# Performance work log

Measured on AMD Instinct MI355X. Metric: run time of the kernel, lower is better.

Reference implementation:

```python
import jax, jax.numpy as jnp
import numpy as np

N, IN_DIM, NUM_HEADS, HEAD_DIM = 8192, 256, 4, 64
NEG_SLOPE = 0.2


def setup_inputs() -> dict:
    key = jax.random.key(0)
    k1, k2, k3, k4 = jax.random.split(key, 4)
    h = jax.random.normal(k1, (N, IN_DIM), dtype=jnp.float32)
    adj = jax.random.randint(k2, (N, N), 0, 2, dtype=jnp.int32)
    # xavier-ish init scale for the per-head projection weights and attention vector
    W = jax.random.normal(k3, (NUM_HEADS, IN_DIM, HEAD_DIM), dtype=jnp.float32) * (1.0 / np.sqrt(IN_DIM))
    a = jax.random.normal(k4, (2 * HEAD_DIM, 1), dtype=jnp.float32) * (1.0 / np.sqrt(2 * HEAD_DIM))
    return {"h": h, "adj": adj, "W": W, "a": a}


def reference(h, adj, W, a):
    # Wh: (H, N, D) -- per-head linear projection (no bias)
    Wh = jnp.einsum('ni,hid->hnd', h, W)
    # torch computes cat([Wh_i, Wh_j]) @ a; equivalent decomposition:
    # e_ij = (Wh_i . a[:D]) + (Wh_j . a[D:])  -- avoids the O(N^2 * 2D) concat tensor
    a1 = a[:HEAD_DIM, 0]  # (D,)
    a2 = a[HEAD_DIM:, 0]  # (D,)
    s_i = jnp.einsum('hnd,d->hn', Wh, a1)  # (H, N)
    s_j = jnp.einsum('hnd,d->hn', Wh, a2)  # (H, N)
    e = s_i[:, :, None] + s_j[:, None, :]  # (H, N, N)
    e = jnp.where(e > 0, e, NEG_SLOPE * e)  # leaky_relu(0.2)
    e = jnp.where(adj[None, :, :] == 0, -jnp.inf, e)
    att = jax.nn.softmax(e, axis=-1)  # torch softmax(dim=1) over last axis of (N,N)
    # dropout is identity in eval mode
    out = jnp.einsum('hnm,hmd->hnd', att, Wh)  # (H, N, D)
    # concat head outputs along feature dim -> (N, H*D)
    return jnp.transpose(out, (1, 0, 2)).reshape(N, NUM_HEADS * HEAD_DIM)
```

## Files before the change

kernel.cpp:

```cpp
#include <hip/hip_runtime.h>
#include <hip/hip_bf16.h>

#define NND 8192

typedef __attribute__((ext_vector_type(8))) __bf16 bf16x8;
typedef __attribute__((ext_vector_type(4))) float f32x4;
typedef __attribute__((ext_vector_type(4))) unsigned int u32x4;
typedef __attribute__((ext_vector_type(2))) unsigned int u32x2;

__global__ __launch_bounds__(256) void gat_phase0(
    const int* __restrict__ adj, unsigned long long* __restrict__ bits)
{
  const int wave = threadIdx.x >> 6, lane = threadIdx.x & 63;
  const int row = blockIdx.x * 4 + wave;
  const int* ap = adj + (size_t)row * NND + lane;
  unsigned long long* bp = bits + (size_t)row * 128;
  #pragma unroll 4
  for (int it = 0; it < 128; ++it) {
    int v = ap[it * 64];
    unsigned long long m = __ballot(v != 0);
    if (lane == 0) bp[it] = m;
  }
}

__global__ __launch_bounds__(256) void gat_phase1a(
    const float* __restrict__ W, const float* __restrict__ av,
    float* __restrict__ q1, float* __restrict__ q2)
{
  const int t = blockIdx.x * 256 + threadIdx.x;
  const float* wp = W + (size_t)t * 64;
  float p1 = 0.f, p2 = 0.f;
  #pragma unroll
  for (int d = 0; d < 64; d += 4) {
    f32x4 w  = *(const f32x4*)(wp + d);
    f32x4 a1 = *(const f32x4*)(av + d);
    f32x4 a2 = *(const f32x4*)(av + 64 + d);
    p1 += w[0]*a1[0] + w[1]*a1[1] + w[2]*a1[2] + w[3]*a1[3];
    p2 += w[0]*a2[0] + w[1]*a2[1] + w[2]*a2[2] + w[3]*a2[3];
  }
  q1[t] = p1 * 1.4426950408889634f;
  q2[t] = p2 * 1.4426950408889634f;
}

__global__ __launch_bounds__(1024) void gat_phase1(
    const float* __restrict__ hin, const float* __restrict__ W,
    const float* __restrict__ q1, const float* __restrict__ q2,
    float* __restrict__ s1, float* __restrict__ s2, unsigned int* __restrict__ whbF)
{
  const int t = threadIdx.x;
  const int wave = t >> 6, lane = t & 63;
  const int head = wave & 3, dt = wave >> 2;
  const int lo = lane & 15, kg = lane >> 4;
  const float* Wp = W + head * 16384 + dt * 16 + lo;
  bf16x8 wf[8];
  #pragma unroll
  for (int ks = 0; ks < 8; ++ks)
    #pragma unroll
    for (int e = 0; e < 8; ++e)
      wf[ks][e] = (__bf16)Wp[(ks * 32 + kg * 8 + e) * 64];
  const float* q1h = q1 + head * 256;
  const float* q2h = q2 + head * 256;

  #pragma unroll
  for (int c = 0; c < 2; ++c) {
    const int n0 = blockIdx.x * 32 + c * 16;
    const float* hrow = hin + (size_t)(n0 + lo) * 256;
    f32x4 acc = (f32x4)(0.f);
    float p1 = 0.f, p2 = 0.f;
    #pragma unroll
    for (int ks = 0; ks < 8; ++ks) {
      const int kb = ks * 32 + kg * 8;
      f32x4 h0 = *(const f32x4*)(hrow + kb);
      f32x4 h1 = *(const f32x4*)(hrow + kb + 4);
      bf16x8 hf;
      #pragma unroll
      for (int e = 0; e < 4; ++e) { hf[e] = (__bf16)h0[e]; hf[e + 4] = (__bf16)h1[e]; }
      acc = __builtin_amdgcn_mfma_f32_16x16x32_bf16(hf, wf[ks], acc, 0, 0, 0);
      if (dt == 0) {
        f32x4 qa = *(const f32x4*)(q1h + kb);
        f32x4 qb = *(const f32x4*)(q1h + kb + 4);
        f32x4 qc = *(const f32x4*)(q2h + kb);
        f32x4 qd = *(const f32x4*)(q2h + kb + 4);
        #pragma unroll
        for (int e = 0; e < 4; ++e) {
          p1 = fmaf(h0[e], qa[e], p1); p1 = fmaf(h1[e], qb[e], p1);
          p2 = fmaf(h0[e], qc[e], p2); p2 = fmaf(h1[e], qd[e], p2);
        }
      }
    }
    const int jtg = n0 >> 6, sub = (n0 >> 4) & 3;
    const int chunk = ((head * 4 + dt) * 128 + jtg) * 2 + (kg >> 1);
    unsigned short b0 = __builtin_bit_cast(unsigned short, (__bf16)acc[0]);
    unsigned short b1 = __builtin_bit_cast(unsigned short, (__bf16)acc[1]);
    unsigned short b2 = __builtin_bit_cast(unsigned short, (__bf16)acc[2]);
    unsigned short b3 = __builtin_bit_cast(unsigned short, (__bf16)acc[3]);
    u32x2 wv; wv[0] = (unsigned)b0 | ((unsigned)b1 << 16);
    wv[1] = (unsigned)b2 | ((unsigned)b3 << 16);
    *(u32x2*)(whbF + (size_t)chunk * 256 + (sub * 16 + lo) * 4 + (kg & 1) * 2) = wv;
    if (dt == 0) {
      p1 += __shfl_xor(p1, 16, 64); p1 += __shfl_xor(p1, 32, 64);
      p2 += __shfl_xor(p2, 16, 64); p2 += __shfl_xor(p2, 32, 64);
      if (kg == 0) { s1[head * NND + n0 + lo] = p1; s2[head * NND + n0 + lo] = p2; }
    }
  }
}

__global__ __launch_bounds__(1024) void gat_phase2(
    const unsigned long long* __restrict__ bits, const float* __restrict__ s1,
    const float* __restrict__ s2, const unsigned short* __restrict__ whbF,
    float* __restrict__ out)
{
  __shared__ float red[4][64][44];
  const int t = threadIdx.x;
  const int wave = t >> 6, lane = t & 63;
  const int head = wave & 3, jseg = wave >> 2;
  const int i0 = blockIdx.x * 32;
  const int lo = lane & 15, kg = lane >> 4;
  const float s1v0 = s1[head * NND + i0 + lo];
  const float s1v1 = s1[head * NND + i0 + 16 + lo];
  const unsigned char* br0 = (const unsigned char*)bits + (size_t)(i0 + lo) * 1024 + kg * 2;
  const unsigned char* br1 = br0 + 16 * 1024;
  const float* s2h = s2 + head * NND;
  const char* wfb = (const char*)whbF + (size_t)head * 1048576 + (size_t)lane * 16;
  f32x4 acc0[4], acc1[4], dn0 = (f32x4)(0.f), dn1 = (f32x4)(0.f);
  #pragma unroll
  for (int dt = 0; dt < 4; ++dt) { acc0[dt] = (f32x4)(0.f); acc1[dt] = (f32x4)(0.f); }
  bf16x8 ones;
  #pragma unroll
  for (int e = 0; e < 8; ++e) ones[e] = (__bf16)1.0f;

  auto mkaf = [&](float s1v, unsigned m, f32x4 sa, f32x4 sb, int bb) -> bf16x8 {
    bf16x8 af;
    #pragma unroll
    for (int e = 0; e < 4; ++e) {
      float x = s1v + sa[e];
      x = fmaxf(x, 0.2f * x);
      float w = __builtin_amdgcn_exp2f(x);
      w = ((m >> (bb + e)) & 1u) ? w : 0.0f;
      af[e] = (__bf16)w;
    }
    #pragma unroll
    for (int e = 0; e < 4; ++e) {
      float x = s1v + sb[e];
      x = fmaxf(x, 0.2f * x);
      float w = __builtin_amdgcn_exp2f(x);
      w = ((m >> (bb + 4 + e)) & 1u) ? w : 0.0f;
      af[e + 4] = (__bf16)w;
    }
    return af;
  };

  #pragma unroll 2
  for (int jt = 0; jt < 32; ++jt) {
    const int jtg = jseg * 32 + jt;
    const int j0 = jtg * 64;
    u32x4 bb[8];
    #pragma unroll
    for (int dt = 0; dt < 4; ++dt)
      #pragma unroll
      for (int ks = 0; ks < 2; ++ks)
        bb[dt * 2 + ks] = *(const u32x4*)(wfb + dt * 262144 + jtg * 2048 + ks * 1024);
    const unsigned m0 = *(const unsigned short*)(br0 + (j0 >> 3));
    const unsigned m1 = *(const unsigned short*)(br1 + (j0 >> 3));
    const f32x4 sv0 = *(const f32x4*)(s2h + j0 + kg * 16);
    const f32x4 sv1 = *(const f32x4*)(s2h + j0 + kg * 16 + 4);
    const f32x4 sv2 = *(const f32x4*)(s2h + j0 + kg * 16 + 8);
    const f32x4 sv3 = *(const f32x4*)(s2h + j0 + kg * 16 + 12);
    {
      bf16x8 af = mkaf(s1v0, m0, sv0, sv1, 0);
      acc0[0] = __builtin_amdgcn_mfma_f32_16x16x32_bf16(af, __builtin_bit_cast(bf16x8, bb[0]), acc0[0], 0, 0, 0);
      acc0[1] = __builtin_amdgcn_mfma_f32_16x16x32_bf16(af, __builtin_bit_cast(bf16x8, bb[2]), acc0[1], 0, 0, 0);
      acc0[2] = __builtin_amdgcn_mfma_f32_16x16x32_bf16(af, __builtin_bit_cast(bf16x8, bb[4]), acc0[2], 0, 0, 0);
      acc0[3] = __builtin_amdgcn_mfma_f32_16x16x32_bf16(af, __builtin_bit_cast(bf16x8, bb[6]), acc0[3], 0, 0, 0);
      dn0 = __builtin_amdgcn_mfma_f32_16x16x32_bf16(af, ones, dn0, 0, 0, 0);
      af = mkaf(s1v0, m0, sv2, sv3, 8);
      acc0[0] = __builtin_amdgcn_mfma_f32_16x16x32_bf16(af, __builtin_bit_cast(bf16x8, bb[1]), acc0[0], 0, 0, 0);
      acc0[1] = __builtin_amdgcn_mfma_f32_16x16x32_bf16(af, __builtin_bit_cast(bf16x8, bb[3]), acc0[1], 0, 0, 0);
      acc0[2] = __builtin_amdgcn_mfma_f32_16x16x32_bf16(af, __builtin_bit_cast(bf16x8, bb[5]), acc0[2], 0, 0, 0);
      acc0[3] = __builtin_amdgcn_mfma_f32_16x16x32_bf16(af, __builtin_bit_cast(bf16x8, bb[7]), acc0[3], 0, 0, 0);
      dn0 = __builtin_amdgcn_mfma_f32_16x16x32_bf16(af, ones, dn0, 0, 0, 0);
    }
    {
      bf16x8 af = mkaf(s1v1, m1, sv0, sv1, 0);
      acc1[0] = __builtin_amdgcn_mfma_f32_16x16x32_bf16(af, __builtin_bit_cast(bf16x8, bb[0]), acc1[0], 0, 0, 0);
      acc1[1] = __builtin_amdgcn_mfma_f32_16x16x32_bf16(af, __builtin_bit_cast(bf16x8, bb[2]), acc1[1], 0, 0, 0);
      acc1[2] = __builtin_amdgcn_mfma_f32_16x16x32_bf16(af, __builtin_bit_cast(bf16x8, bb[4]), acc1[2], 0, 0, 0);
      acc1[3] = __builtin_amdgcn_mfma_f32_16x16x32_bf16(af, __builtin_bit_cast(bf16x8, bb[6]), acc1[3], 0, 0, 0);
      dn1 = __builtin_amdgcn_mfma_f32_16x16x32_bf16(af, ones, dn1, 0, 0, 0);
      af = mkaf(s1v1, m1, sv2, sv3, 8);
      acc1[0] = __builtin_amdgcn_mfma_f32_16x16x32_bf16(af, __builtin_bit_cast(bf16x8, bb[1]), acc1[0], 0, 0, 0);
      acc1[1] = __builtin_amdgcn_mfma_f32_16x16x32_bf16(af, __builtin_bit_cast(bf16x8, bb[3]), acc1[1], 0, 0, 0);
      acc1[2] = __builtin_amdgcn_mfma_f32_16x16x32_bf16(af, __builtin_bit_cast(bf16x8, bb[5]), acc1[2], 0, 0, 0);
      acc1[3] = __builtin_amdgcn_mfma_f32_16x16x32_bf16(af, __builtin_bit_cast(bf16x8, bb[7]), acc1[3], 0, 0, 0);
      dn1 = __builtin_amdgcn_mfma_f32_16x16x32_bf16(af, ones, dn1, 0, 0, 0);
    }
  }

  for (int s = 1; s <= 3; ++s) {
    if (jseg == s) {
      #pragma unroll
      for (int dt = 0; dt < 4; ++dt) {
        *(f32x4*)&red[head][lane][dt * 4] = acc0[dt];
        *(f32x4*)&red[head][lane][16 + dt * 4] = acc1[dt];
      }
      *(f32x4*)&red[head][lane][32] = dn0;
      *(f32x4*)&red[head][lane][36] = dn1;
    }
    __syncthreads();
    if (jseg == 0) {
      #pragma unroll
      for (int dt = 0; dt < 4; ++dt) {
        acc0[dt] += *(const f32x4*)&red[head][lane][dt * 4];
        acc1[dt] += *(const f32x4*)&red[head][lane][16 + dt * 4];
      }
      dn0 += *(const f32x4*)&red[head][lane][32];
      dn1 += *(const f32x4*)&red[head][lane][36];
    }
    __syncthreads();
  }
  if (jseg != 0) return;

  #pragma unroll
  for (int r = 0; r < 4; ++r) {
    const float rc0 = 1.0f / dn0[r], rc1 = 1.0f / dn1[r];
    float* op0 = out + (size_t)(i0 + kg * 4 + r) * 256 + head * 64 + lo;
    float* op1 = op0 + 16 * 256;
    #pragma unroll
    for (int dt = 0; dt < 4; ++dt) {
      op0[dt * 16] = acc0[dt][r] * rc0;
      op1[dt * 16] = acc1[dt][r] * rc1;
    }
  }
}

extern "C" void kernel_launch(void* const* d_in, const int* in_sizes, int n_in,
                              void* d_out, int out_size, void* d_ws, size_t ws_size,
                              hipStream_t stream) {
  const float* h   = (const float*)d_in[0];
  const int*   adj = (const int*)d_in[1];
  const float* W   = (const float*)d_in[2];
  const float* a   = (const float*)d_in[3];
  float* out = (float*)d_out;
  float* s1 = (float*)d_ws;
  float* s2 = s1 + 4 * NND;
  float* q1 = s2 + 4 * NND;
  float* q2 = q1 + 1024;
  unsigned long long* bits = (unsigned long long*)(q2 + 1024);
  unsigned int* whbF = (unsigned int*)(bits + (size_t)NND * 128);
  gat_phase0<<<dim3(NND / 4), dim3(256), 0, stream>>>(adj, bits);
  gat_phase1a<<<dim3(4), dim3(256), 0, stream>>>(W, a, q1, q2);
  gat_phase1<<<dim3(NND / 32), dim3(1024), 0, stream>>>(h, W, q1, q2, s1, s2, whbF);
  gat_phase2<<<dim3(NND / 32), dim3(1024), 0, stream>>>(bits, s1, s2, (const unsigned short*)whbF, out);
}
```

Before: 564.4 us.

## Remove split-j reduction in attention kernel, add register double-buffering, rework projection

The attention kernel no longer splits the neighbor dimension across four wave groups and reduces partial sums through shared memory. Each wave now handles 16 rows over all 8192 columns with a software-pipelined double buffer of register tiles, and blocks shrink to 512 threads. This removes the LDS reduction and barriers and halves per-wave accumulator registers, but each wave now loops four times longer and the masks and Wh tiles are reloaded per 16-row group instead of shared across 32 rows. The projection kernel is also reorganized: one wave per head computes all four feature tiles from register-held h fragments, and blocks shrink to 256 threads.

After: 542.1 us. -4.0%, faster.

```diff
diff --git a/kernel.cpp b/kernel.cpp
--- a/kernel.cpp
+++ b/kernel.cpp
@@ -42,53 +42,55 @@
   q2[t] = p2 * 1.4426950408889634f;
 }
 
-__global__ __launch_bounds__(1024) void gat_phase1(
+__global__ __launch_bounds__(256) void gat_phase1(
     const float* __restrict__ hin, const float* __restrict__ W,
     const float* __restrict__ q1, const float* __restrict__ q2,
     float* __restrict__ s1, float* __restrict__ s2, unsigned int* __restrict__ whbF)
 {
   const int t = threadIdx.x;
-  const int wave = t >> 6, lane = t & 63;
-  const int head = wave & 3, dt = wave >> 2;
+  const int head = t >> 6, lane = t & 63;
   const int lo = lane & 15, kg = lane >> 4;
-  const float* Wp = W + head * 16384 + dt * 16 + lo;
-  bf16x8 wf[8];
-  #pragma unroll
-  for (int ks = 0; ks < 8; ++ks)
-    #pragma unroll
-    for (int e = 0; e < 8; ++e)
-      wf[ks][e] = (__bf16)Wp[(ks * 32 + kg * 8 + e) * 64];
+  const int n0 = blockIdx.x * 16;
+  const float* hrow = hin + (size_t)(n0 + lo) * 256;
   const float* q1h = q1 + head * 256;
   const float* q2h = q2 + head * 256;
-
-  #pragma unroll
-  for (int c = 0; c < 2; ++c) {
-    const int n0 = blockIdx.x * 32 + c * 16;
-    const float* hrow = hin + (size_t)(n0 + lo) * 256;
+  bf16x8 hf[8];
+  float p1 = 0.f, p2 = 0.f;
+  #pragma unroll
+  for (int ks = 0; ks < 8; ++ks) {
+    const int kb = ks * 32 + kg * 8;
+    f32x4 h0 = *(const f32x4*)(hrow + kb);
+    f32x4 h1 = *(const f32x4*)(hrow + kb + 4);
+    #pragma unroll
+    for (int e = 0; e < 4; ++e) { hf[ks][e] = (__bf16)h0[e]; hf[ks][e + 4] = (__bf16)h1[e]; }
+    f32x4 qa = *(const f32x4*)(q1h + kb);
+    f32x4 qb = *(const f32x4*)(q1h + kb + 4);
+    f32x4 qc = *(const f32x4*)(q2h + kb);
+    f32x4 qd = *(const f32x4*)(q2h + kb + 4);
+    #pragma unroll
+    for (int e = 0; e < 4; ++e) {
+      p1 = fmaf(h0[e], qa[e], p1); p1 = fmaf(h1[e], qb[e], p1);
+      p2 = fmaf(h0[e], qc[e], p2); p2 = fmaf(h1[e], qd[e], p2);
+    }
+  }
+  p1 += __shfl_xor(p1, 16, 64); p1 += __shfl_xor(p1, 32, 64);
+  p2 += __shfl_xor(p2, 16, 64); p2 += __shfl_xor(p2, 32, 64);
+  if (kg == 0) { s1[head * NND + n0 + lo] = p1; s2[head * NND + n0 + lo] = p2; }
+
+  const int jtg = n0 >> 6, sub = (n0 >> 4) & 3;
+  #pragma unroll
+  for (int dt = 0; dt < 4; ++dt) {
+    const float* Wp = W + head * 16384 + dt * 16 + lo;
     f32x4 acc = (f32x4)(0.f);
-    float p1 = 0.f, p2 = 0.f;
     #pragma unroll
     for (int ks = 0; ks < 8; ++ks) {
       const int kb = ks * 32 + kg * 8;
-      f32x4 h0 = *(const f32x4*)(hrow + kb);
-      f32x4 h1 = *(const f32x4*)(hrow + kb + 4);
-      bf16x8 hf;
+      bf16x8 wf;
       #pragma unroll
-      for (int e = 0; e < 4; ++e) { hf[e] = (__bf16)h0[e]; hf[e + 4] = (__bf16)h1[e]; }
-      acc = __builtin_amdgcn_mfma_f32_16x16x32_bf16(hf, wf[ks], acc, 0, 0, 0);
-      if (dt == 0) {
-        f32x4 qa = *(const f32x4*)(q1h + kb);
-        f32x4 qb = *(const f32x4*)(q1h + kb + 4);
-        f32x4 qc = *(const f32x4*)(q2h + kb);
-        f32x4 qd = *(const f32x4*)(q2h + kb + 4);
-        #pragma unroll
-        for (int e = 0; e < 4; ++e) {
-          p1 = fmaf(h0[e], qa[e], p1); p1 = fmaf(h1[e], qb[e], p1);
-          p2 = fmaf(h0[e], qc[e], p2); p2 = fmaf(h1[e], qd[e], p2);
-        }
-      }
-    }
-    const int jtg = n0 >> 6, sub = (n0 >> 4) & 3;
+      for (int e = 0; e < 8; ++e)
+        wf[e] = (__bf16)Wp[(kb + e) * 64];
+      acc = __builtin_amdgcn_mfma_f32_16x16x32_bf16(hf[ks], wf, acc, 0, 0, 0);
+    }
     const int chunk = ((head * 4 + dt) * 128 + jtg) * 2 + (kg >> 1);
     unsigned short b0 = __builtin_bit_cast(unsigned short, (__bf16)acc[0]);
     unsigned short b1 = __builtin_bit_cast(unsigned short, (__bf16)acc[1]);
@@ -97,39 +99,31 @@
     u32x2 wv; wv[0] = (unsigned)b0 | ((unsigned)b1 << 16);
     wv[1] = (unsigned)b2 | ((unsigned)b3 << 16);
     *(u32x2*)(whbF + (size_t)chunk * 256 + (sub * 16 + lo) * 4 + (kg & 1) * 2) = wv;
-    if (dt == 0) {
-      p1 += __shfl_xor(p1, 16, 64); p1 += __shfl_xor(p1, 32, 64);
-      p2 += __shfl_xor(p2, 16, 64); p2 += __shfl_xor(p2, 32, 64);
-      if (kg == 0) { s1[head * NND + n0 + lo] = p1; s2[head * NND + n0 + lo] = p2; }
-    }
-  }
-}
-
-__global__ __launch_bounds__(1024) void gat_phase2(
+  }
+}
+
+__global__ __launch_bounds__(512) void gat_phase2(
     const unsigned long long* __restrict__ bits, const float* __restrict__ s1,
     const float* __restrict__ s2, const unsigned short* __restrict__ whbF,
     float* __restrict__ out)
 {
-  __shared__ float red[4][64][44];
   const int t = threadIdx.x;
   const int wave = t >> 6, lane = t & 63;
-  const int head = wave & 3, jseg = wave >> 2;
-  const int i0 = blockIdx.x * 32;
+  const int head = wave & 3, rg = wave >> 2;
+  const int i0 = blockIdx.x * 32 + rg * 16;
   const int lo = lane & 15, kg = lane >> 4;
-  const float s1v0 = s1[head * NND + i0 + lo];
-  const float s1v1 = s1[head * NND + i0 + 16 + lo];
-  const unsigned char* br0 = (const unsigned char*)bits + (size_t)(i0 + lo) * 1024 + kg * 2;
-  const unsigned char* br1 = br0 + 16 * 1024;
+  const float s1v = s1[head * NND + i0 + lo];
+  const unsigned char* br = (const unsigned char*)bits + (size_t)(i0 + lo) * 1024 + kg * 2;
   const float* s2h = s2 + head * NND;
   const char* wfb = (const char*)whbF + (size_t)head * 1048576 + (size_t)lane * 16;
-  f32x4 acc0[4], acc1[4], dn0 = (f32x4)(0.f), dn1 = (f32x4)(0.f);
-  #pragma unroll
-  for (int dt = 0; dt < 4; ++dt) { acc0[dt] = (f32x4)(0.f); acc1[dt] = (f32x4)(0.f); }
+  f32x4 acc[4], dn = (f32x4)(0.f);
+  #pragma unroll
+  for (int dt = 0; dt < 4; ++dt) acc[dt] = (f32x4)(0.f);
   bf16x8 ones;
   #pragma unroll
   for (int e = 0; e < 8; ++e) ones[e] = (__bf16)1.0f;
 
-  auto mkaf = [&](float s1v, unsigned m, f32x4 sa, f32x4 sb, int bb) -> bf16x8 {
+  auto mkaf = [&](unsigned m, f32x4 sa, f32x4 sb, int bb) -> bf16x8 {
     bf16x8 af;
     #pragma unroll
     for (int e = 0; e < 4; ++e) {
@@ -150,86 +144,57 @@
     return af;
   };
 
-  #pragma unroll 2
-  for (int jt = 0; jt < 32; ++jt) {
-    const int jtg = jseg * 32 + jt;
-    const int j0 = jtg * 64;
-    u32x4 bb[8];
+  auto LOADT = [&](u32x4 (&bb)[8], f32x4 (&sv)[4], unsigned& m, int jtg) {
     #pragma unroll
     for (int dt = 0; dt < 4; ++dt)
       #pragma unroll
       for (int ks = 0; ks < 2; ++ks)
         bb[dt * 2 + ks] = *(const u32x4*)(wfb + dt * 262144 + jtg * 2048 + ks * 1024);
-    const unsigned m0 = *(const unsigned short*)(br0 + (j0 >> 3));
-    const unsigned m1 = *(const unsigned short*)(br1 + (j0 >> 3));
-    const f32x4 sv0 = *(const f32x4*)(s2h + j0 + kg * 16);
-    const f32x4 sv1 = *(const f32x4*)(s2h + j0 + kg * 16 + 4);
-    const f32x4 sv2 = *(const f32x4*)(s2h + j0 + kg * 16 + 8);
-    const f32x4 sv3 = *(const f32x4*)(s2h + j0 + kg * 16 + 12);
-    {
-      bf16x8 af = mkaf(s1v0, m0, sv0, sv1, 0);
-      acc0[0] = __builtin_amdgcn_mfma_f32_16x16x32_bf16(af, __builtin_bit_cast(bf16x8, bb[0]), acc0[0], 0, 0, 0);
-      acc0[1] = __builtin_amdgcn_mfma_f32_16x16x32_bf16(af, __builtin_bit_cast(bf16x8, bb[2]), acc0[1], 0, 0, 0);
-      acc0[2] = __builtin_amdgcn_mfma_f32_16x16x32_bf16(af, __builtin_bit_cast(bf16x8, bb[4]), acc0[2], 0, 0, 0);
-      acc0[3] = __builtin_amdgcn_mfma_f32_16x16x32_bf16(af, __builtin_bit_cast(bf16x8, bb[6]), acc0[3], 0, 0, 0);
-      dn0 = __builtin_amdgcn_mfma_f32_16x16x32_bf16(af, ones, dn0, 0, 0, 0);
-      af = mkaf(s1v0, m0, sv2, sv3, 8);
-      acc0[0] = __builtin_amdgcn_mfma_f32_16x16x32_bf16(af, __builtin_bit_cast(bf16x8, bb[1]), acc0[0], 0, 0, 0);
-      acc0[1] = __builtin_amdgcn_mfma_f32_16x16x32_bf16(af, __builtin_bit_cast(bf16x8, bb[3]), acc0[1], 0, 0, 0);
-      acc0[2] = __builtin_amdgcn_mfma_f32_16x16x32_bf16(af, __builtin_bit_cast(bf16x8, bb[5]), acc0[2], 0, 0, 0);
-      acc0[3] = __builtin_amdgcn_mfma_f32_16x16x32_bf16(af, __builtin_bit_cast(bf16x8, bb[7]), acc0[3], 0, 0, 0);
-      dn0 = __builtin_amdgcn_mfma_f32_16x16x32_bf16(af, ones, dn0, 0, 0, 0);
-    }
-    {
-      bf16x8 af = mkaf(s1v1, m1, sv0, sv1, 0);
-      acc1[0] = __builtin_amdgcn_mfma_f32_16x16x32_bf16(af, __builtin_bit_cast(bf16x8, bb[0]), acc1[0], 0, 0, 0);
-      acc1[1] = __builtin_amdgcn_mfma_f32_16x16x32_bf16(af, __builtin_bit_cast(bf16x8, bb[2]), acc1[1], 0, 0, 0);
-      acc1[2] = __builtin_amdgcn_mfma_f32_16x16x32_bf16(af, __builtin_bit_cast(bf16x8, bb[4]), acc1[2], 0, 0, 0);
-      acc1[3] = __builtin_amdgcn_mfma_f32_16x16x32_bf16(af, __builtin_bit_cast(bf16x8, bb[6]), acc1[3], 0, 0, 0);
-      dn1 = __builtin_amdgcn_mfma_f32_16x16x32_bf16(af, ones, dn1, 0, 0, 0);
-      af = mkaf(s1v1, m1, sv2, sv3, 8);
-      acc1[0] = __builtin_amdgcn_mfma_f32_16x16x32_bf16(af, __builtin_bit_cast(bf16x8, bb[1]), acc1[0], 0, 0, 0);
-      acc1[1] = __builtin_amdgcn_mfma_f32_16x16x32_bf16(af, __builtin_bit_cast(bf16x8, bb[3]), acc1[1], 0, 0, 0);
-      acc1[2] = __builtin_amdgcn_mfma_f32_16x16x32_bf16(af, __builtin_bit_cast(bf16x8, bb[5]), acc1[2], 0, 0, 0);
-      acc1[3] = __builtin_amdgcn_mfma_f32_16x16x32_bf16(af, __builtin_bit_cast(bf16x8, bb[7]), acc1[3], 0, 0, 0);
-      dn1 = __builtin_amdgcn_mfma_f32_16x16x32_bf16(af, ones, dn1, 0, 0, 0);
-    }
-  }
-
-  for (int s = 1; s <= 3; ++s) {
-    if (jseg == s) {
-      #pragma unroll
-      for (int dt = 0; dt < 4; ++dt) {
-        *(f32x4*)&red[head][lane][dt * 4] = acc0[dt];
-        *(f32x4*)&red[head][lane][16 + dt * 4] = acc1[dt];
-      }
-      *(f32x4*)&red[head][lane][32] = dn0;
-      *(f32x4*)&red[head][lane][36] = dn1;
-    }
-    __syncthreads();
-    if (jseg == 0) {
-      #pragma unroll
-      for (int dt = 0; dt < 4; ++dt) {
-        acc0[dt] += *(const f32x4*)&red[head][lane][dt * 4];
-        acc1[dt] += *(const f32x4*)&red[head][lane][16 + dt * 4];
-      }
-      dn0 += *(const f32x4*)&red[head][lane][32];
-      dn1 += *(const f32x4*)&red[head][lane][36];
-    }
-    __syncthreads();
-  }
-  if (jseg != 0) return;
+    m = *(const unsigned short*)(br + jtg * 8);
+    const int j0 = jtg * 64;
+    sv[0] = *(const f32x4*)(s2h + j0 + kg * 16);
+    sv[1] = *(const f32x4*)(s2h + j0 + kg * 16 + 4);
+    sv[2] = *(const f32x4*)(s2h + j0 + kg * 16 + 8);
+    sv[3] = *(const f32x4*)(s2h + j0 + kg * 16 + 12);
+  };
+
+  auto COMP = [&](u32x4 (&bb)[8], f32x4 (&sv)[4], unsigned m) {
+    bf16x8 af = mkaf(m, sv[0], sv[1], 0);
+    acc[0] = __builtin_amdgcn_mfma_f32_16x16x32_bf16(af, __builtin_bit_cast(bf16x8, bb[0]), acc[0], 0, 0, 0);
+    acc[1] = __builtin_amdgcn_mfma_f32_16x16x32_bf16(af, __builtin_bit_cast(bf16x8, bb[2]), acc[1], 0, 0, 0);
+    acc[2] = __builtin_amdgcn_mfma_f32_16x16x32_bf16(af, __builtin_bit_cast(bf16x8, bb[4]), acc[2], 0, 0, 0);
+    acc[3] = __builtin_amdgcn_mfma_f32_16x16x32_bf16(af, __builtin_bit_cast(bf16x8, bb[6]), acc[3], 0, 0, 0);
+    dn = __builtin_amdgcn_mfma_f32_16x16x32_bf16(af, ones, dn, 0, 0, 0);
+    af = mkaf(m, sv[2], sv[3], 8);
+    acc[0] = __builtin_amdgcn_mfma_f32_16x16x32_bf16(af, __builtin_bit_cast(bf16x8, bb[1]), acc[0], 0, 0, 0);
+    acc[1] = __builtin_amdgcn_mfma_f32_16x16x32_bf16(af, __builtin_bit_cast(bf16x8, bb[3]), acc[1], 0, 0, 0);
+    acc[2] = __builtin_amdgcn_mfma_f32_16x16x32_bf16(af, __builtin_bit_cast(bf16x8, bb[5]), acc[2], 0, 0, 0);
+    acc[3] = __builtin_amdgcn_mfma_f32_16x16x32_bf16(af, __builtin_bit_cast(bf16x8, bb[7]), acc[3], 0, 0, 0);
+    dn = __builtin_amdgcn_mfma_f32_16x16x32_bf16(af, ones, dn, 0, 0, 0);
+  };
+
+  u32x4 bbA[8], bbB[8];
+  f32x4 svA[4], svB[4];
+  unsigned mA, mB;
+
+  LOADT(bbA, svA, mA, 0);
+  for (int p = 0; p < 63; ++p) {
+    LOADT(bbB, svB, mB, 2 * p + 1);
+    COMP(bbA, svA, mA);
+    LOADT(bbA, svA, mA, 2 * p + 2);
+    COMP(bbB, svB, mB);
+  }
+  LOADT(bbB, svB, mB, 127);
+  COMP(bbA, svA, mA);
+  COMP(bbB, svB, mB);
 
   #pragma unroll
   for (int r = 0; r < 4; ++r) {
-    const float rc0 = 1.0f / dn0[r], rc1 = 1.0f / dn1[r];
-    float* op0 = out + (size_t)(i0 + kg * 4 + r) * 256 + head * 64 + lo;
-    float* op1 = op0 + 16 * 256;
-    #pragma unroll
-    for (int dt = 0; dt < 4; ++dt) {
-      op0[dt * 16] = acc0[dt][r] * rc0;
-      op1[dt * 16] = acc1[dt][r] * rc1;
-    }
+    const float rc = 1.0f / dn[r];
+    float* op = out + (size_t)(i0 + kg * 4 + r) * 256 + head * 64 + lo;
+    #pragma unroll
+    for (int dt = 0; dt < 4; ++dt)
+      op[dt * 16] = acc[dt][r] * rc;
   }
 }
 
@@ -249,6 +214,6 @@
   unsigned int* whbF = (unsigned int*)(bits + (size_t)NND * 128);
   gat_phase0<<<dim3(NND / 4), dim3(256), 0, stream>>>(adj, bits);
   gat_phase1a<<<dim3(4), dim3(256), 0, stream>>>(W, a, q1, q2);
-  gat_phase1<<<dim3(NND / 32), dim3(1024), 0, stream>>>(h, W, q1, q2, s1, s2, whbF);
-  gat_phase2<<<dim3(NND / 32), dim3(1024), 0, stream>>>(bits, s1, s2, (const unsigned short*)whbF, out);
-}
+  gat_phase1<<<dim3(NND / 16), dim3(256), 0, stream>>>(h, W, q1, q2, s1, s2, whbF);
+  gat_phase2<<<dim3(NND / 32), dim3(512), 0, stream>>>(bits, s1, s2, (const unsigned short*)whbF, out);
+}
```
